# Optimization experiments

Hardware: AMD Instinct MI355X
Metric: run time of the kernel (lower is better)

The kernel has to match this reference:

```python
import jax, jax.numpy as jnp
import numpy as np

NQ = 4
NL = 3
HEADS = 8

_H = jnp.asarray(np.array([[1, 1], [1, -1]], np.complex64) / np.sqrt(2.0))
_X = jnp.asarray(np.array([[0, 1], [1, 0]], np.complex64))
_Y = jnp.asarray(np.array([[0, -1j], [1j, 0]], np.complex64))
_Z = jnp.asarray(np.array([[1, 0], [0, -1]], np.complex64))
_CNOT = jnp.asarray(np.array([[1, 0, 0, 0], [0, 1, 0, 0], [0, 0, 0, 1], [0, 0, 1, 0]], np.complex64))


def _rx(t):
    c = jnp.cos(t / 2).astype(jnp.complex64)
    s = (-1j * jnp.sin(t / 2)).astype(jnp.complex64)
    return jnp.stack([jnp.stack([c, s]), jnp.stack([s, c])])


def _ry(t):
    c = jnp.cos(t / 2).astype(jnp.complex64)
    s = jnp.sin(t / 2).astype(jnp.complex64)
    return jnp.stack([jnp.stack([c, -s]), jnp.stack([s, c])])


def _rz(t):
    e = jnp.exp((-0.5j) * t).astype(jnp.complex64)
    z = jnp.zeros((), jnp.complex64)
    return jnp.stack([jnp.stack([e, z]), jnp.stack([z, jnp.conj(e)])])


def _crx(t):
    # control-RX in |control,target> basis
    return jnp.eye(4, dtype=jnp.complex64).at[2:, 2:].set(_rx(t))


def _ap1(psi, U, q):
    # apply 2x2 gate U on qubit axis q of psi:(2,2,2,2)
    return jnp.moveaxis(jnp.tensordot(U, psi, axes=[[1], [q]]), 0, q)


def _ap2(psi, U, q1, q2):
    p = jnp.moveaxis(psi, (q1, q2), (0, 1)).reshape(4, 4)
    p = (U @ p).reshape(2, 2, 2, 2)
    return jnp.moveaxis(p, (0, 1), (q1, q2))


def _expv(psi, P, q):
    return jnp.real(jnp.vdot(psi, _ap1(psi, P, q)))


def _circuit(inp, w, ew, gam, bet):
    # inp:(4,)  w,ew:(3,4)  gam,bet:(3,)  -> (12,) expvals Z,X,Y
    psi = jnp.zeros((16,), jnp.complex64).at[0].set(1.0).reshape(2, 2, 2, 2)
    for i in range(NQ):  # AngleEmbedding(rotation='Y')
        psi = _ap1(psi, _ry(inp[i]), i)
    for L in range(NL):
        for i in range(NQ):
            psi = _ap1(psi, _rx(w[L, i]), i)
            psi = _ap1(psi, _ry(w[L, i]), i)
            psi = _ap1(psi, _rz(w[L, i]), i)
        for i in range(NQ):  # CRX entangling ring
            psi = _ap2(psi, _crx(ew[L, i]), i, (i + 1) % NQ)
        # Grover diffusion
        for q in range(NQ):
            psi = _ap1(psi, _H, q)
        for q in range(NQ):
            psi = _ap1(psi, _X, q)
        psi = _ap1(psi, _H, NQ - 1)
        psi = psi.at[1, 1, 1, :].set(psi[1, 1, 1, ::-1])  # CCCX ctrl=[0,1,2] tgt=3
        psi = _ap1(psi, _H, NQ - 1)
        for q in range(NQ):
            psi = _ap1(psi, _X, q)
        for q in range(NQ):
            psi = _ap1(psi, _H, q)
        # QAOA cost + mixer
        for i in range(NQ - 1):
            psi = _ap2(psi, _CNOT, i, i + 1)
            psi = _ap1(psi, _rz(gam[L]), i + 1)
            psi = _ap2(psi, _CNOT, i, i + 1)
        for q in range(NQ):
            psi = _ap1(psi, _rx(bet[L]), q)
    meas = [_expv(psi, _Z, q) for q in range(NQ)]
    meas += [_expv(psi, _X, q) for q in range(NQ)]
    meas += [_expv(psi, _Y, q) for q in range(NQ)]
    return jnp.stack(meas)


_vqc = jax.vmap(_circuit, in_axes=(0, None, None, None, None))


def _layernorm(x, g, b, eps=1e-5):
    mu = jnp.mean(x, -1, keepdims=True)
    var = jnp.mean((x - mu) ** 2, -1, keepdims=True)
    return (x - mu) * jax.lax.rsqrt(var + eps) * g + b


def _qtransform(xf, Wp, bp, ln_g, ln_b, w, ew, gam, bet):
    p = jnp.tanh(xf @ Wp.T + bp)  # (BS,4)
    p = _layernorm(p, ln_g, ln_b)
    return _vqc(p, w, ew, gam, bet)  # (BS,12)


def setup_inputs() -> dict:
    key = jax.random.key(0)
    ks = jax.random.split(key, 32)
    B, S, Hd = 4, 1024, 512
    d = {"x": jax.random.normal(ks[0], (B, S, Hd), jnp.float32)}
    d["Wp"] = jax.random.normal(ks[1], (NQ, Hd), jnp.float32) * 0.05
    d["bp"] = jnp.zeros((NQ,), jnp.float32)
    d["ln_g"] = jnp.ones((NQ,), jnp.float32)
    d["ln_b"] = jnp.zeros((NQ,), jnp.float32)
    i = 2
    for pfx in ["q", "k", "v"]:
        d[pfx + "w"] = 0.01 * jax.random.normal(ks[i], (NL, NQ), jnp.float32)
        d[pfx + "e"] = 0.01 * jax.random.normal(ks[i + 1], (NL, NQ), jnp.float32)
        d[pfx + "g"] = 0.01 * jax.random.normal(ks[i + 2], (NL,), jnp.float32)
        d[pfx + "b"] = 0.01 * jax.random.normal(ks[i + 3], (NL,), jnp.float32)
        i += 4
    fused = 3 * NQ
    d["Wq"] = jax.random.normal(ks[i], (Hd, fused), jnp.float32) * 0.2
    d["bq"] = jnp.zeros((Hd,), jnp.float32)
    d["Wk"] = jax.random.normal(ks[i + 1], (Hd, fused), jnp.float32) * 0.2
    d["bk"] = jnp.zeros((Hd,), jnp.float32)
    d["Wv"] = jax.random.normal(ks[i + 2], (Hd, fused), jnp.float32) * 0.2
    d["bv"] = jnp.zeros((Hd,), jnp.float32)
    d["Wo"] = jax.random.normal(ks[i + 3], (Hd, Hd), jnp.float32) * 0.05
    d["bo"] = jnp.zeros((Hd,), jnp.float32)
    return d


def reference(x, Wp, bp, ln_g, ln_b, qw, qe, qg, qb, kw, ke, kg, kb, vw, ve, vg, vb,
              Wq, bq, Wk, bk, Wv, bv, Wo, bo):
    B, S, Hd = x.shape
    hd = Hd // HEADS
    xf = x.reshape(B * S, Hd)
    tq = _qtransform(xf, Wp, bp, ln_g, ln_b, qw, qe, qg, qb)
    tk = _qtransform(xf, Wp, bp, ln_g, ln_b, kw, ke, kg, kb)
    tv = _qtransform(xf, Wp, bp, ln_g, ln_b, vw, ve, vg, vb)
    q = (tq @ Wq.T + bq).reshape(B, S, HEADS, hd)
    k = (tk @ Wk.T + bk).reshape(B, S, HEADS, hd)
    v = (tv @ Wv.T + bv).reshape(B, S, HEADS, hd)
    scale = float(hd) ** 0.5
    attn = jax.nn.softmax(jnp.einsum('bqhd,bkhd->bhqk', q, k) / scale, axis=-1)
    out = jnp.einsum('bhqk,bkhd->bqhd', attn, v).reshape(B, S, Hd)
    return out @ Wo.T + bo
```

## Files before the change

kernel.cpp:

```cpp
#include <hip/hip_runtime.h>
#include <hip/hip_bf16.h>
#include <math.h>

#define NROWS 4096
#define HD 512
#define HEADS 8
#define HDD 64
#define SEQ 1024
#define QSCALE 0.18033688011112042f

typedef unsigned short u16;
typedef __attribute__((ext_vector_type(8))) short sh8;
typedef __attribute__((ext_vector_type(4))) float f4;

__device__ __forceinline__ f4 mfma16(sh8 a, sh8 b, f4 c) {
  return __builtin_amdgcn_mfma_f32_16x16x32_bf16(a, b, c, 0, 0, 0);
}

__device__ __forceinline__ u16 f2bf(float x) {
  union { float f; unsigned u; } v; v.f = x;
  unsigned r = v.u + 0x7fff + ((v.u >> 16) & 1);
  return (u16)(r >> 16);
}

#define SWZA(r, cb) ((((r) * 128) + (cb)) ^ (((r) & 7) << 4))
#define SWZB(r, cb) ((((r) * 256) + (cb)) ^ (((r) & 7) << 4))

__global__ __launch_bounds__(256) void k_prep(
    const float* __restrict__ qw, const float* __restrict__ qe,
    const float* __restrict__ qg, const float* __restrict__ qb,
    const float* __restrict__ kw, const float* __restrict__ ke,
    const float* __restrict__ kg, const float* __restrict__ kb,
    const float* __restrict__ vw, const float* __restrict__ ve,
    const float* __restrict__ vg, const float* __restrict__ vb,
    float* __restrict__ Mout) {
  const int c = blockIdx.x;
  const int tid = threadIdx.x;
  __shared__ float aC[32], aS[32];
  __shared__ float GT[60][8];
  __shared__ int   GM[60][2];
  __shared__ float PF[3][16][2];
  __shared__ float SR[16][17], SI[16][17];
  __shared__ float TS[16], TI[16];
  __shared__ float Ur[256], Ui[256];

  const float* w = (c == 0) ? qw : (c == 1) ? kw : vw;
  const float* e = (c == 0) ? qe : (c == 1) ? ke : ve;
  const float* g = (c == 0) ? qg : (c == 1) ? kg : vg;
  const float* b = (c == 0) ? qb : (c == 1) ? kb : vb;

  if (tid < 30) {
    float ang = (tid < 12) ? w[tid] : (tid < 24) ? e[tid - 12]
               : (tid < 27) ? g[tid - 24] : b[tid - 27];
    float s_, c_;
    sincosf(0.5f * ang, &s_, &c_);
    aC[tid] = c_; aS[tid] = s_;
  }
  __syncthreads();

  if (tid < 60) {
    int L = tid / 20, s5 = tid % 20;
    int typ, aidx, M, C;
    if (s5 < 12) {
      int q = s5 / 3; typ = s5 % 3; aidx = L * 4 + q; M = 8 >> q; C = 0;
    } else if (s5 < 16) {
      int q = s5 - 12; typ = 0; aidx = 12 + L * 4 + q;
      C = 8 >> q; M = 8 >> ((q + 1) & 3);
    } else {
      int q = s5 - 16; typ = 0; aidx = 27 + L; M = 8 >> q; C = 0;
    }
    float cc = aC[aidx], ss = aS[aidx];
    float u0r = cc, u0i = 0.f, u1r = 0.f, u1i = 0.f,
          u2r = 0.f, u2i = 0.f, u3r = cc, u3i = 0.f;
    if (typ == 0)      { u1i = -ss; u2i = -ss; }
    else if (typ == 1) { u1r = -ss; u2r = ss; }
    else               { u0i = -ss; u3i = ss; }
    GT[tid][0] = u0r; GT[tid][1] = u0i; GT[tid][2] = u1r; GT[tid][3] = u1i;
    GT[tid][4] = u2r; GT[tid][5] = u2i; GT[tid][6] = u3r; GT[tid][7] = u3i;
    GM[tid][0] = M; GM[tid][1] = C;
  }
  if (tid >= 64 && tid < 112) {
    int idx = tid - 64, L = idx >> 4, a = idx & 15;
    float cg = aC[24 + L], sg = aS[24 + L];
    float c2 = cg * cg - sg * sg, s2 = 2.f * cg * sg;
    float c3 = cg * c2 - sg * s2, s3 = cg * s2 + sg * c2;
    int u = (a ^ (a >> 1)) & 7;
    int n = (u & 1) + ((u >> 1) & 1) + ((u >> 2) & 1);
    PF[L][a][0] = (n == 0 || n == 3) ? c3 : cg;
    PF[L][a][1] = (n == 0) ? -s3 : (n == 1) ? -sg : (n == 2) ? sg : s3;
  }
  for (int i = tid; i < 256; i += 256) {
    SR[i >> 4][i & 15] = (i >> 4) == (i & 15) ? 1.f : 0.f;
    SI[i >> 4][i & 15] = 0.f;
  }
  __syncthreads();

  const int p = tid >> 4, col = tid & 15;
  for (int L = 0; L < 3; ++L) {
    for (int s5 = 0; s5 < 16; ++s5) {
      if (tid < 128) {
        int gi = L * 20 + s5;
        const float* u = GT[gi];
        int M = GM[gi][0], C = GM[gi][1];
        int lo = p & (M - 1);
        int a = ((p - lo) << 1) | lo;
        int bb = a | M;
        bool act = (C == 0) | ((a & C) != 0);
        float ar = SR[a][col], ai = SI[a][col];
        float br = SR[bb][col], bi = SI[bb][col];
        float nar = u[0]*ar - u[1]*ai + u[2]*br - u[3]*bi;
        float nai = u[0]*ai + u[1]*ar + u[2]*bi + u[3]*br;
        float nbr = u[4]*ar - u[5]*ai + u[6]*br - u[7]*bi;
        float nbi = u[4]*ai + u[5]*ar + u[6]*bi + u[7]*br;
        SR[a][col]  = act ? nar : ar;  SI[a][col]  = act ? nai : ai;
        SR[bb][col] = act ? nbr : br;  SI[bb][col] = act ? nbi : bi;
      }
      __syncthreads();
    }
    if (tid < 16) {
      float sR = 0.f, sI = 0.f;
      for (int a = 0; a < 16; ++a) { sR += SR[a][tid]; sI += SI[a][tid]; }
      TS[tid] = sR * 0.125f; TI[tid] = sI * 0.125f;
    }
    __syncthreads();
    if (tid < 128) {
      for (int k = 0; k < 2; ++k) {
        int a = 2 * p + k;
        float vr = SR[a][col] - TS[col];
        float vi = SI[a][col] - TI[col];
        float pc = PF[L][a][0], ps = PF[L][a][1];
        SR[a][col] = vr * pc - vi * ps;
        SI[a][col] = vr * ps + vi * pc;
      }
    }
    __syncthreads();
    for (int s5 = 16; s5 < 20; ++s5) {
      if (tid < 128) {
        int gi = L * 20 + s5;
        const float* u = GT[gi];
        int M = GM[gi][0];
        int lo = p & (M - 1);
        int a = ((p - lo) << 1) | lo;
        int bb = a | M;
        float ar = SR[a][col], ai = SI[a][col];
        float br = SR[bb][col], bi = SI[bb][col];
        SR[a][col]  = u[0]*ar - u[1]*ai + u[2]*br - u[3]*bi;
        SI[a][col]  = u[0]*ai + u[1]*ar + u[2]*bi + u[3]*br;
        SR[bb][col] = u[4]*ar - u[5]*ai + u[6]*br - u[7]*bi;
        SI[bb][col] = u[4]*ai + u[5]*ar + u[6]*bi + u[7]*br;
      }
      __syncthreads();
    }
  }

  for (int i = tid; i < 256; i += 256) {
    Ur[i] = SR[i >> 4][i & 15];
    Ui[i] = SI[i >> 4][i & 15];
  }
  __syncthreads();

  if (tid < 192) {
    const int j = tid >> 4, a = tid & 15;
    const int typ = j >> 2;
    const int Mm = 8 >> (j & 3);
    float ax[4] = {0.f,0.f,0.f,0.f}, ay[4] = {0.f,0.f,0.f,0.f},
          az[4] = {0.f,0.f,0.f,0.f}, aw[4] = {0.f,0.f,0.f,0.f};
#pragma clang loop unroll_count(4)
    for (int k = 0; k < 16; ++k) {
      float uar = Ur[k * 16 + a], uai = Ui[k * 16 + a];
      int k2; float cR, cI;
      if (typ == 0)      { k2 = k;      float z = (k & Mm) ? -1.f : 1.f; cR = z*uar; cI = z*uai; }
      else if (typ == 1) { k2 = k ^ Mm; cR = uar; cI = uai; }
      else               { k2 = k ^ Mm; float sg = (k & Mm) ? 1.f : -1.f; cR = sg*uai; cI = -sg*uar; }
      const float* ur2 = Ur + k2 * 16;
      const float* ui2 = Ui + k2 * 16;
#pragma unroll
      for (int i = 0; i < 4; ++i) {
        ax[i] += cR * ur2[i*4+0] + cI * ui2[i*4+0];
        ay[i] += cR * ur2[i*4+1] + cI * ui2[i*4+1];
        az[i] += cR * ur2[i*4+2] + cI * ui2[i*4+2];
        aw[i] += cR * ur2[i*4+3] + cI * ui2[i*4+3];
      }
    }
    float* dst = Mout + ((c * 12 + j) * 16 + a) * 16;
#pragma unroll
    for (int i = 0; i < 4; ++i)
      ((float4*)dst)[i] = make_float4(ax[i], ay[i], az[i], aw[i]);
  }
}

__global__ __launch_bounds__(256) void k_fused(const float* __restrict__ x,
    const float* __restrict__ Wp, const float* __restrict__ bp,
    const float* __restrict__ ln_g, const float* __restrict__ ln_b,
    const float* __restrict__ Mg,
    const float* __restrict__ Wq, const float* __restrict__ bq,
    const float* __restrict__ Wk, const float* __restrict__ bk,
    const float* __restrict__ Wv, const float* __restrict__ bv,
    u16* __restrict__ Qo, u16* __restrict__ Ko, u16* __restrict__ Vto) {
  const int rb = blockIdx.x;
  const int tid = threadIdx.x;
  __shared__ float Ml[3][12][256];
  __shared__ float pl[16][4];
  __shared__ float psil[16][17];
  __shared__ float tt[3][16][12];

  {
    const float4* src = (const float4*)Mg;
    float4* dst = (float4*)&Ml[0][0][0];
    for (int i = tid; i < 2304; i += 256) dst[i] = src[i];
  }

  const int w = tid >> 6, lane = tid & 63;
  {
    float4 wpa[4], wpb[4];
#pragma unroll
    for (int j = 0; j < 4; ++j) {
      wpa[j] = *(const float4*)(Wp + j * HD + lane * 8);
      wpb[j] = *(const float4*)(Wp + j * HD + lane * 8 + 4);
    }
    for (int i = 0; i < 4; ++i) {
      int r = w * 4 + i;
      const float* xr = x + (rb * 16 + r) * HD + lane * 8;
      float4 xa = *(const float4*)xr, xb = *(const float4*)(xr + 4);
      float acc[4];
#pragma unroll
      for (int j = 0; j < 4; ++j)
        acc[j] = xa.x*wpa[j].x + xa.y*wpa[j].y + xa.z*wpa[j].z + xa.w*wpa[j].w
               + xb.x*wpb[j].x + xb.y*wpb[j].y + xb.z*wpb[j].z + xb.w*wpb[j].w;
#pragma unroll
      for (int j = 0; j < 4; ++j)
#pragma unroll
        for (int off = 32; off >= 1; off >>= 1)
          acc[j] += __shfl_xor(acc[j], off);
      if (lane == 0) {
        float v0 = tanhf(acc[0] + bp[0]);
        float v1 = tanhf(acc[1] + bp[1]);
        float v2 = tanhf(acc[2] + bp[2]);
        float v3 = tanhf(acc[3] + bp[3]);
        float mu = 0.25f * (v0 + v1 + v2 + v3);
        float d0 = v0 - mu, d1 = v1 - mu, d2 = v2 - mu, d3 = v3 - mu;
        float inv = rsqrtf(0.25f * (d0*d0 + d1*d1 + d2*d2 + d3*d3) + 1e-5f);
        pl[r][0] = d0 * inv * ln_g[0] + ln_b[0];
        pl[r][1] = d1 * inv * ln_g[1] + ln_b[1];
        pl[r][2] = d2 * inv * ln_g[2] + ln_b[2];
        pl[r][3] = d3 * inv * ln_g[3] + ln_b[3];
      }
    }
  }
  __syncthreads();

  if (tid < 16) {
    float cs[4], sn[4];
    sincosf(0.5f * pl[tid][0], &sn[0], &cs[0]);
    sincosf(0.5f * pl[tid][1], &sn[1], &cs[1]);
    sincosf(0.5f * pl[tid][2], &sn[2], &cs[2]);
    sincosf(0.5f * pl[tid][3], &sn[3], &cs[3]);
    float q01[4] = {cs[0]*cs[1], cs[0]*sn[1], sn[0]*cs[1], sn[0]*sn[1]};
    float q23[4] = {cs[2]*cs[3], cs[2]*sn[3], sn[2]*cs[3], sn[2]*sn[3]};
#pragma unroll
    for (int a = 0; a < 16; ++a) psil[tid][a] = q01[a >> 2] * q23[a & 3];
  }
  __syncthreads();

  if (tid < 192) {
    const int r = tid & 15, j = tid >> 4;
    float psi[16];
#pragma unroll
    for (int a = 0; a < 16; ++a) psi[a] = psil[r][a];
#pragma clang loop unroll(disable)
    for (int c = 0; c < 3; ++c) {
      const float* Mj = &Ml[c][j][0];
      float y = 0.f;
#pragma unroll
      for (int a = 0; a < 16; ++a) {
        float rsum = 0.f;
#pragma unroll
        for (int i = 0; i < 16; ++i) rsum += Mj[a*16+i] * psi[i];
        y += psi[a] * rsum;
      }
      tt[c][r][j] = y;
    }
  }
  __syncthreads();

  const int n0 = rb * 16, b = n0 >> 10, ss0 = n0 & 1023;
  {
    const int o0 = tid * 2;
    float wq0[12], wq1[12], wk0[12], wk1[12];
#pragma unroll
    for (int j = 0; j < 12; ++j) {
      wq0[j] = Wq[o0*12 + j];  wq1[j] = Wq[(o0+1)*12 + j];
      wk0[j] = Wk[o0*12 + j];  wk1[j] = Wk[(o0+1)*12 + j];
    }
    const float bq0 = bq[o0], bq1 = bq[o0+1], bk0 = bk[o0], bk1 = bk[o0+1];
    const int h = o0 >> 6, d = o0 & 63;
    u16* qrow = Qo + ((b * HEADS + h) * SEQ + ss0) * HDD + d;
    u16* krow = Ko + ((b * HEADS + h) * SEQ + ss0) * HDD + d;
    for (int rr = 0; rr < 16; ++rr) {
      float a0 = bq0, a1 = bq1, c0 = bk0, c1 = bk1;
#pragma unroll
      for (int j = 0; j < 12; ++j) {
        float tq = tt[0][rr][j], tk = tt[1][rr][j];
        a0 += tq * wq0[j]; a1 += tq * wq1[j];
        c0 += tk * wk0[j]; c1 += tk * wk1[j];
      }
      unsigned qv = (unsigned)f2bf(a0 * QSCALE) | ((unsigned)f2bf(a1 * QSCALE) << 16);
      unsigned kv = (unsigned)f2bf(c0) | ((unsigned)f2bf(c1) << 16);
      *(unsigned*)(qrow + rr * HDD) = qv;
      *(unsigned*)(krow + rr * HDD) = kv;
    }
  }
  {
    const int sp = tid & 7, gg = tid >> 3;
    const int r0 = 2 * sp, r1 = r0 + 1;
    for (int i = 0; i < 16; ++i) {
      int o = gg + 32 * i;
      float v0 = bv[o], v1 = bv[o];
#pragma unroll
      for (int j = 0; j < 12; ++j) {
        float wv = Wv[o * 12 + j];
        v0 += tt[2][r0][j] * wv;
        v1 += tt[2][r1][j] * wv;
      }
      unsigned vv = (unsigned)f2bf(v0) | ((unsigned)f2bf(v1) << 16);
      *(unsigned*)(Vto + (b * 512 + o) * SEQ + ss0 + r0) = vv;
    }
  }
}

__global__ __launch_bounds__(256) void k_attn_mfma(const u16* __restrict__ Q,
    const u16* __restrict__ K, const u16* __restrict__ Vt,
    u16* __restrict__ Ob) {
  const int bh = blockIdx.y, qt = blockIdx.x;
  const int tid = threadIdx.x, w = tid >> 6, l = tid & 63;
  const int lr = l & 15, lh = l >> 4;

  __shared__ u16 Kl[2][128 * 64];
  __shared__ u16 Vl[2][64 * 128];
  __shared__ u16 Pl[4][16 * 128];

  const u16* Qb = Q + (bh * SEQ + qt * 64) * HDD;
  const u16* Kb = K + bh * SEQ * HDD;
  const u16* Vb = Vt + bh * HDD * SEQ;

  sh8 qf[2];
#pragma unroll
  for (int kk = 0; kk < 2; ++kk)
    qf[kk] = *(const sh8*)(Qb + (w * 16 + lr) * HDD + kk * 32 + lh * 8);

  f4 oacc[4];
  float lsum[4] = {0.f, 0.f, 0.f, 0.f};
#pragma unroll
  for (int n = 0; n < 4; ++n) oacc[n] = (f4){0.f, 0.f, 0.f, 0.f};

  sh8 kreg[4], vreg[4];

#define STAGE_LOAD(ch) { \
    _Pragma("unroll") \
    for (int i = 0; i < 4; ++i) { \
      int idx = i * 256 + tid; \
      kreg[i] = *(const sh8*)(Kb + ((ch) * 128 + (idx >> 3)) * HDD + (idx & 7) * 8); \
      vreg[i] = *(const sh8*)(Vb + (idx >> 4) * SEQ + (ch) * 128 + (idx & 15) * 8); \
    } }
#define STAGE_WRITE(buf) { \
    _Pragma("unroll") \
    for (int i = 0; i < 4; ++i) { \
      int idx = i * 256 + tid; \
      *(sh8*)((char*)Kl[buf] + SWZA(idx >> 3, (idx & 7) * 16)) = kreg[i]; \
      *(sh8*)((char*)Vl[buf] + SWZB(idx >> 4, (idx & 15) * 16)) = vreg[i]; \
    } }

  STAGE_LOAD(0)
  STAGE_WRITE(0)
  __syncthreads();

  for (int ch = 0; ch < SEQ / 128; ++ch) {
    const int cur = ch & 1;
    if (ch < 7) STAGE_LOAD(ch + 1)

    f4 sacc[8];
#pragma unroll
    for (int n = 0; n < 8; ++n) sacc[n] = (f4){0.f, 0.f, 0.f, 0.f};
#pragma unroll
    for (int kk = 0; kk < 2; ++kk) {
#pragma unroll
      for (int n = 0; n < 8; ++n) {
        sh8 kf = *(const sh8*)((const char*)Kl[cur] + SWZA(n * 16 + lr, kk * 64 + lh * 16));
        sacc[n] = mfma16(qf[kk], kf, sacc[n]);
      }
    }

#pragma unroll
    for (int n = 0; n < 8; ++n) {
#pragma unroll
      for (int r = 0; r < 4; ++r) {
        float pv = exp2f(sacc[n][r]);
        lsum[r] += pv;
        *(u16*)((char*)Pl[w] + SWZB(lh * 4 + r, (n * 16 + lr) * 2)) = f2bf(pv);
      }
    }

#pragma unroll
    for (int kk = 0; kk < 4; ++kk) {
      sh8 pf = *(const sh8*)((const char*)Pl[w] + SWZB(lr, kk * 64 + lh * 16));
#pragma unroll
      for (int n = 0; n < 4; ++n) {
        sh8 vf = *(const sh8*)((const char*)Vl[cur] + SWZB(n * 16 + lr, kk * 64 + lh * 16));
        oacc[n] = mfma16(pf, vf, oacc[n]);
      }
    }

    if (ch < 7) STAGE_WRITE(cur ^ 1)
    __syncthreads();
  }
#undef STAGE_LOAD
#undef STAGE_WRITE

#pragma unroll
  for (int r = 0; r < 4; ++r) {
    lsum[r] += __shfl_xor(lsum[r], 1); lsum[r] += __shfl_xor(lsum[r], 2);
    lsum[r] += __shfl_xor(lsum[r], 4); lsum[r] += __shfl_xor(lsum[r], 8);
  }

  int bb = bh >> 3, h = bh & 7;
#pragma unroll
  for (int r = 0; r < 4; ++r) {
    int row = qt * 64 + w * 16 + lh * 4 + r;
    float inv = 1.f / lsum[r];
#pragma unroll
    for (int n = 0; n < 4; ++n)
      Ob[(bb * SEQ + row) * HD + h * 64 + n * 16 + lr] = f2bf(oacc[n][r] * inv);
  }
}

__global__ __launch_bounds__(256) void k_oproj_mfma(const u16* __restrict__ A,
    const float* __restrict__ W, const float* __restrict__ bo,
    float* __restrict__ out) {
  const int nb = blockIdx.x, ob = blockIdx.y;
  const int tid = threadIdx.x, w = tid >> 6, l = tid & 63;
  const int lr = l & 15, lh = l >> 4;
  __shared__ u16 Al[64 * 64];
  __shared__ u16 Wl[64 * 64];
  f4 acc[4];
#pragma unroll
  for (int n = 0; n < 4; ++n) acc[n] = (f4){0.f, 0.f, 0.f, 0.f};
  for (int ch = 0; ch < 8; ++ch) {
    __syncthreads();
#pragma unroll
    for (int i = 0; i < 2; ++i) {
      int idx = i * 256 + tid;
      int r = idx >> 3, c8 = idx & 7;
      *(sh8*)((char*)Al + SWZA(r, c8 * 16)) =
          *(const sh8*)(A + (nb * 64 + r) * HD + ch * 64 + c8 * 8);
      const float* wp = W + (ob * 64 + r) * HD + ch * 64 + c8 * 8;
      float4 f0 = *(const float4*)wp;
      float4 f1 = *(const float4*)(wp + 4);
      sh8 wv;
      wv[0] = (short)f2bf(f0.x); wv[1] = (short)f2bf(f0.y);
      wv[2] = (short)f2bf(f0.z); wv[3] = (short)f2bf(f0.w);
      wv[4] = (short)f2bf(f1.x); wv[5] = (short)f2bf(f1.y);
      wv[6] = (short)f2bf(f1.z); wv[7] = (short)f2bf(f1.w);
      *(sh8*)((char*)Wl + SWZA(r, c8 * 16)) = wv;
    }
    __syncthreads();
#pragma unroll
    for (int kk = 0; kk < 2; ++kk) {
      sh8 af = *(const sh8*)((const char*)Al + SWZA(w * 16 + lr, kk * 64 + lh * 16));
#pragma unroll
      for (int n = 0; n < 4; ++n) {
        sh8 wf = *(const sh8*)((const char*)Wl + SWZA(n * 16 + lr, kk * 64 + lh * 16));
        acc[n] = mfma16(af, wf, acc[n]);
      }
    }
  }
#pragma unroll
  for (int r = 0; r < 4; ++r) {
    int row = nb * 64 + w * 16 + lh * 4 + r;
#pragma unroll
    for (int n = 0; n < 4; ++n) {
      int col = ob * 64 + n * 16 + lr;
      out[row * HD + col] = acc[n][r] + bo[col];
    }
  }
}

extern "C" void kernel_launch(void* const* d_in, const int* in_sizes, int n_in,
                              void* d_out, int out_size, void* d_ws, size_t ws_size,
                              hipStream_t stream) {
  const float* x    = (const float*)d_in[0];
  const float* Wp   = (const float*)d_in[1];
  const float* bp   = (const float*)d_in[2];
  const float* ln_g = (const float*)d_in[3];
  const float* ln_b = (const float*)d_in[4];
  const float* qw   = (const float*)d_in[5];
  const float* qe   = (const float*)d_in[6];
  const float* qg   = (const float*)d_in[7];
  const float* qb_  = (const float*)d_in[8];
  const float* kw   = (const float*)d_in[9];
  const float* ke   = (const float*)d_in[10];
  const float* kg   = (const float*)d_in[11];
  const float* kb_  = (const float*)d_in[12];
  const float* vw   = (const float*)d_in[13];
  const float* ve   = (const float*)d_in[14];
  const float* vg   = (const float*)d_in[15];
  const float* vb_  = (const float*)d_in[16];
  const float* Wq   = (const float*)d_in[17];
  const float* bq   = (const float*)d_in[18];
  const float* Wk   = (const float*)d_in[19];
  const float* bk   = (const float*)d_in[20];
  const float* Wv   = (const float*)d_in[21];
  const float* bv   = (const float*)d_in[22];
  const float* Wo   = (const float*)d_in[23];
  const float* bo   = (const float*)d_in[24];

  float* ws   = (float*)d_ws;
  float* Mbuf = ws;
  u16* qb  = (u16*)(Mbuf + 9216);
  u16* kb  = qb + 32 * SEQ * HDD;
  u16* vtb = kb + 32 * SEQ * HDD;
  u16* ab  = vtb + 32 * SEQ * HDD;

  k_prep<<<3, 256, 0, stream>>>(qw, qe, qg, qb_, kw, ke, kg, kb_,
                                vw, ve, vg, vb_, Mbuf);
  k_fused<<<NROWS / 16, 256, 0, stream>>>(x, Wp, bp, ln_g, ln_b, Mbuf,
                                          Wq, bq, Wk, bk, Wv, bv, qb, kb, vtb);
  dim3 ga(SEQ / 64, 32);
  k_attn_mfma<<<ga, 256, 0, stream>>>(qb, kb, vtb, ab);
  dim3 go(NROWS / 64, HD / 64);
  k_oproj_mfma<<<go, 256, 0, stream>>>(ab, Wo, bo, (float*)d_out);
}
```

Before: 86.42 us.

## Shrink front-end row tiles and restructure attention to read K/V from global

The front kernel now handles 4 rows per block instead of 16. It reads the circuit matrices straight from global memory instead of staging 36KB in LDS, and spreads the 3 circuits across threads. Q/K/V projections use vectorized weight loads, and V is written as packed 64-bit stores. The attention kernel gives each wave 32 query rows (two 16-row MFMA tiles sharing K/V fragments), so the grid halves. It drops LDS double-buffering of K/V in favour of direct global/cache loads, separated only by sched barriers. This removes LDS staging and block syncs at the cost of more global/L2 traffic and higher register pressure.

```diff
diff --git a/kernel.cpp b/kernel.cpp
--- a/kernel.cpp
+++ b/kernel.cpp
@@ -10,6 +10,8 @@
 #define QSCALE 0.18033688011112042f
 
 typedef unsigned short u16;
+typedef unsigned int u32;
+typedef unsigned long long u64;
 typedef __attribute__((ext_vector_type(8))) short sh8;
 typedef __attribute__((ext_vector_type(4))) float f4;
 
@@ -189,7 +191,7 @@
   }
 }
 
-__global__ __launch_bounds__(256) void k_fused(const float* __restrict__ x,
+__global__ __launch_bounds__(256) void k_front(const float* __restrict__ x,
     const float* __restrict__ Wp, const float* __restrict__ bp,
     const float* __restrict__ ln_g, const float* __restrict__ ln_b,
     const float* __restrict__ Mg,
@@ -199,57 +201,44 @@
     u16* __restrict__ Qo, u16* __restrict__ Ko, u16* __restrict__ Vto) {
   const int rb = blockIdx.x;
   const int tid = threadIdx.x;
-  __shared__ float Ml[3][12][256];
-  __shared__ float pl[16][4];
-  __shared__ float psil[16][17];
-  __shared__ float tt[3][16][12];
+  const int w = tid >> 6, lane = tid & 63;
+  __shared__ float pl[4][4];
+  __shared__ float psil[4][16];
+  __shared__ float tt[3][4][12];
 
   {
-    const float4* src = (const float4*)Mg;
-    float4* dst = (float4*)&Ml[0][0][0];
-    for (int i = tid; i < 2304; i += 256) dst[i] = src[i];
-  }
-
-  const int w = tid >> 6, lane = tid & 63;
-  {
-    float4 wpa[4], wpb[4];
+    const float* xr = x + (rb * 4 + w) * HD + lane * 8;
+    float4 xa = *(const float4*)xr, xb = *(const float4*)(xr + 4);
+    float acc[4];
 #pragma unroll
     for (int j = 0; j < 4; ++j) {
-      wpa[j] = *(const float4*)(Wp + j * HD + lane * 8);
-      wpb[j] = *(const float4*)(Wp + j * HD + lane * 8 + 4);
-    }
-    for (int i = 0; i < 4; ++i) {
-      int r = w * 4 + i;
-      const float* xr = x + (rb * 16 + r) * HD + lane * 8;
-      float4 xa = *(const float4*)xr, xb = *(const float4*)(xr + 4);
-      float acc[4];
-#pragma unroll
-      for (int j = 0; j < 4; ++j)
-        acc[j] = xa.x*wpa[j].x + xa.y*wpa[j].y + xa.z*wpa[j].z + xa.w*wpa[j].w
-               + xb.x*wpb[j].x + xb.y*wpb[j].y + xb.z*wpb[j].z + xb.w*wpb[j].w;
-#pragma unroll
-      for (int j = 0; j < 4; ++j)
-#pragma unroll
-        for (int off = 32; off >= 1; off >>= 1)
-          acc[j] += __shfl_xor(acc[j], off);
-      if (lane == 0) {
-        float v0 = tanhf(acc[0] + bp[0]);
-        float v1 = tanhf(acc[1] + bp[1]);
-        float v2 = tanhf(acc[2] + bp[2]);
-        float v3 = tanhf(acc[3] + bp[3]);
-        float mu = 0.25f * (v0 + v1 + v2 + v3);
-        float d0 = v0 - mu, d1 = v1 - mu, d2 = v2 - mu, d3 = v3 - mu;
-        float inv = rsqrtf(0.25f * (d0*d0 + d1*d1 + d2*d2 + d3*d3) + 1e-5f);
-        pl[r][0] = d0 * inv * ln_g[0] + ln_b[0];
-        pl[r][1] = d1 * inv * ln_g[1] + ln_b[1];
-        pl[r][2] = d2 * inv * ln_g[2] + ln_b[2];
-        pl[r][3] = d3 * inv * ln_g[3] + ln_b[3];
-      }
+      const float* wr = Wp + j * HD + lane * 8;
+      float4 wa = *(const float4*)wr, wb = *(const float4*)(wr + 4);
+      acc[j] = xa.x*wa.x + xa.y*wa.y + xa.z*wa.z + xa.w*wa.w
+             + xb.x*wb.x + xb.y*wb.y + xb.z*wb.z + xb.w*wb.w;
+    }
+#pragma unroll
+    for (int j = 0; j < 4; ++j)
+#pragma unroll
+      for (int off = 32; off >= 1; off >>= 1)
+        acc[j] += __shfl_xor(acc[j], off);
+    if (lane == 0) {
+      float v0 = tanhf(acc[0] + bp[0]);
+      float v1 = tanhf(acc[1] + bp[1]);
+      float v2 = tanhf(acc[2] + bp[2]);
+      float v3 = tanhf(acc[3] + bp[3]);
+      float mu = 0.25f * (v0 + v1 + v2 + v3);
+      float d0 = v0 - mu, d1 = v1 - mu, d2 = v2 - mu, d3 = v3 - mu;
+      float inv = rsqrtf(0.25f * (d0*d0 + d1*d1 + d2*d2 + d3*d3) + 1e-5f);
+      pl[w][0] = d0 * inv * ln_g[0] + ln_b[0];
+      pl[w][1] = d1 * inv * ln_g[1] + ln_b[1];
+      pl[w][2] = d2 * inv * ln_g[2] + ln_b[2];
+      pl[w][3] = d3 * inv * ln_g[3] + ln_b[3];
     }
   }
   __syncthreads();
 
-  if (tid < 16) {
+  if (tid < 4) {
     float cs[4], sn[4];
     sincosf(0.5f * pl[tid][0], &sn[0], &cs[0]);
     sincosf(0.5f * pl[tid][1], &sn[1], &cs[1]);
@@ -262,175 +251,169 @@
   }
   __syncthreads();
 
-  if (tid < 192) {
-    const int r = tid & 15, j = tid >> 4;
+  if (tid < 144) {
+    const int c = tid / 48, rem = tid - c * 48, j = rem >> 2, r = rem & 3;
     float psi[16];
 #pragma unroll
     for (int a = 0; a < 16; ++a) psi[a] = psil[r][a];
-#pragma clang loop unroll(disable)
-    for (int c = 0; c < 3; ++c) {
-      const float* Mj = &Ml[c][j][0];
-      float y = 0.f;
-#pragma unroll
-      for (int a = 0; a < 16; ++a) {
-        float rsum = 0.f;
-#pragma unroll
-        for (int i = 0; i < 16; ++i) rsum += Mj[a*16+i] * psi[i];
-        y += psi[a] * rsum;
-      }
-      tt[c][r][j] = y;
-    }
+    const float4* Mj = (const float4*)(Mg + (c * 12 + j) * 256);
+    float y = 0.f;
+#pragma unroll
+    for (int a = 0; a < 16; ++a) {
+      float rsum = 0.f;
+#pragma unroll
+      for (int i = 0; i < 4; ++i) {
+        float4 m4 = Mj[a * 4 + i];
+        rsum += m4.x*psi[i*4] + m4.y*psi[i*4+1] + m4.z*psi[i*4+2] + m4.w*psi[i*4+3];
+      }
+      y += psi[a] * rsum;
+    }
+    tt[c][r][j] = y;
   }
   __syncthreads();
 
-  const int n0 = rb * 16, b = n0 >> 10, ss0 = n0 & 1023;
-  {
-    const int o0 = tid * 2;
-    float wq0[12], wq1[12], wk0[12], wk1[12];
-#pragma unroll
-    for (int j = 0; j < 12; ++j) {
-      wq0[j] = Wq[o0*12 + j];  wq1[j] = Wq[(o0+1)*12 + j];
-      wk0[j] = Wk[o0*12 + j];  wk1[j] = Wk[(o0+1)*12 + j];
-    }
-    const float bq0 = bq[o0], bq1 = bq[o0+1], bk0 = bk[o0], bk1 = bk[o0+1];
-    const int h = o0 >> 6, d = o0 & 63;
-    u16* qrow = Qo + ((b * HEADS + h) * SEQ + ss0) * HDD + d;
-    u16* krow = Ko + ((b * HEADS + h) * SEQ + ss0) * HDD + d;
-    for (int rr = 0; rr < 16; ++rr) {
-      float a0 = bq0, a1 = bq1, c0 = bk0, c1 = bk1;
-#pragma unroll
-      for (int j = 0; j < 12; ++j) {
-        float tq = tt[0][rr][j], tk = tt[1][rr][j];
-        a0 += tq * wq0[j]; a1 += tq * wq1[j];
-        c0 += tk * wk0[j]; c1 += tk * wk1[j];
-      }
-      unsigned qv = (unsigned)f2bf(a0 * QSCALE) | ((unsigned)f2bf(a1 * QSCALE) << 16);
-      unsigned kv = (unsigned)f2bf(c0) | ((unsigned)f2bf(c1) << 16);
-      *(unsigned*)(qrow + rr * HDD) = qv;
-      *(unsigned*)(krow + rr * HDD) = kv;
-    }
-  }
-  {
-    const int sp = tid & 7, gg = tid >> 3;
-    const int r0 = 2 * sp, r1 = r0 + 1;
-    for (int i = 0; i < 16; ++i) {
-      int o = gg + 32 * i;
-      float v0 = bv[o], v1 = bv[o];
-#pragma unroll
-      for (int j = 0; j < 12; ++j) {
-        float wv = Wv[o * 12 + j];
-        v0 += tt[2][r0][j] * wv;
-        v1 += tt[2][r1][j] * wv;
-      }
-      unsigned vv = (unsigned)f2bf(v0) | ((unsigned)f2bf(v1) << 16);
-      *(unsigned*)(Vto + (b * 512 + o) * SEQ + ss0 + r0) = vv;
-    }
-  }
-}
-
-__global__ __launch_bounds__(256) void k_attn_mfma(const u16* __restrict__ Q,
+  const int o0 = tid * 2;
+  const int b = rb >> 8, ss0 = (rb & 255) * 4;
+  const int h = o0 >> 6, d = o0 & 63;
+#pragma unroll
+  for (int c = 0; c < 3; ++c) {
+    const float* W  = (c == 0) ? Wq : (c == 1) ? Wk : Wv;
+    const float* bb = (c == 0) ? bq : (c == 1) ? bk : bv;
+    float4 w0a = *(const float4*)(W + o0 * 12);
+    float4 w0b = *(const float4*)(W + o0 * 12 + 4);
+    float4 w0c = *(const float4*)(W + o0 * 12 + 8);
+    float4 w1a = *(const float4*)(W + o0 * 12 + 12);
+    float4 w1b = *(const float4*)(W + o0 * 12 + 16);
+    float4 w1c = *(const float4*)(W + o0 * 12 + 20);
+    float b0 = bb[o0], b1 = bb[o0 + 1];
+    float r0[4], r1[4];
+#pragma unroll
+    for (int r = 0; r < 4; ++r) {
+      const float* t = tt[c][r];
+      r0[r] = b0 + t[0]*w0a.x + t[1]*w0a.y + t[2]*w0a.z + t[3]*w0a.w
+                 + t[4]*w0b.x + t[5]*w0b.y + t[6]*w0b.z + t[7]*w0b.w
+                 + t[8]*w0c.x + t[9]*w0c.y + t[10]*w0c.z + t[11]*w0c.w;
+      r1[r] = b1 + t[0]*w1a.x + t[1]*w1a.y + t[2]*w1a.z + t[3]*w1a.w
+                 + t[4]*w1b.x + t[5]*w1b.y + t[6]*w1b.z + t[7]*w1b.w
+                 + t[8]*w1c.x + t[9]*w1c.y + t[10]*w1c.z + t[11]*w1c.w;
+    }
+    if (c == 0) {
+      u16* qrow = Qo + ((b * HEADS + h) * SEQ + ss0) * HDD + d;
+#pragma unroll
+      for (int r = 0; r < 4; ++r)
+        *(u32*)(qrow + r * HDD) =
+            (u32)f2bf(r0[r] * QSCALE) | ((u32)f2bf(r1[r] * QSCALE) << 16);
+    } else if (c == 1) {
+      u16* krow = Ko + ((b * HEADS + h) * SEQ + ss0) * HDD + d;
+#pragma unroll
+      for (int r = 0; r < 4; ++r)
+        *(u32*)(krow + r * HDD) = (u32)f2bf(r0[r]) | ((u32)f2bf(r1[r]) << 16);
+    } else {
+      u64 v0 = (u64)((u32)f2bf(r0[0]) | ((u32)f2bf(r0[1]) << 16)) |
+               ((u64)((u32)f2bf(r0[2]) | ((u32)f2bf(r0[3]) << 16)) << 32);
+      u64 v1 = (u64)((u32)f2bf(r1[0]) | ((u32)f2bf(r1[1]) << 16)) |
+               ((u64)((u32)f2bf(r1[2]) | ((u32)f2bf(r1[3]) << 16)) << 32);
+      *(u64*)(Vto + (b * 512 + o0) * SEQ + ss0) = v0;
+      *(u64*)(Vto + (b * 512 + o0 + 1) * SEQ + ss0) = v1;
+    }
+  }
+}
+
+__global__ __launch_bounds__(256) void k_attn(const u16* __restrict__ Q,
     const u16* __restrict__ K, const u16* __restrict__ Vt,
     u16* __restrict__ Ob) {
   const int bh = blockIdx.y, qt = blockIdx.x;
   const int tid = threadIdx.x, w = tid >> 6, l = tid & 63;
   const int lr = l & 15, lh = l >> 4;
 
-  __shared__ u16 Kl[2][128 * 64];
-  __shared__ u16 Vl[2][64 * 128];
-  __shared__ u16 Pl[4][16 * 128];
-
-  const u16* Qb = Q + (bh * SEQ + qt * 64) * HDD;
+  __shared__ u16 Pl[4][32 * 128];
+
+  const u16* Qb = Q + (bh * SEQ + qt * 128 + w * 32) * HDD;
   const u16* Kb = K + bh * SEQ * HDD;
   const u16* Vb = Vt + bh * HDD * SEQ;
-
-  sh8 qf[2];
-#pragma unroll
-  for (int kk = 0; kk < 2; ++kk)
-    qf[kk] = *(const sh8*)(Qb + (w * 16 + lr) * HDD + kk * 32 + lh * 8);
-
-  f4 oacc[4];
-  float lsum[4] = {0.f, 0.f, 0.f, 0.f};
-#pragma unroll
-  for (int n = 0; n < 4; ++n) oacc[n] = (f4){0.f, 0.f, 0.f, 0.f};
-
-  sh8 kreg[4], vreg[4];
-
-#define STAGE_LOAD(ch) { \
-    _Pragma("unroll") \
-    for (int i = 0; i < 4; ++i) { \
-      int idx = i * 256 + tid; \
-      kreg[i] = *(const sh8*)(Kb + ((ch) * 128 + (idx >> 3)) * HDD + (idx & 7) * 8); \
-      vreg[i] = *(const sh8*)(Vb + (idx >> 4) * SEQ + (ch) * 128 + (idx & 15) * 8); \
-    } }
-#define STAGE_WRITE(buf) { \
-    _Pragma("unroll") \
-    for (int i = 0; i < 4; ++i) { \
-      int idx = i * 256 + tid; \
-      *(sh8*)((char*)Kl[buf] + SWZA(idx >> 3, (idx & 7) * 16)) = kreg[i]; \
-      *(sh8*)((char*)Vl[buf] + SWZB(idx >> 4, (idx & 15) * 16)) = vreg[i]; \
-    } }
-
-  STAGE_LOAD(0)
-  STAGE_WRITE(0)
-  __syncthreads();
+  u16* Plw = Pl[w];
+
+  sh8 qf[2][2];
+#pragma unroll
+  for (int m = 0; m < 2; ++m)
+#pragma unroll
+    for (int kk = 0; kk < 2; ++kk)
+      qf[m][kk] = *(const sh8*)(Qb + (m * 16 + lr) * HDD + kk * 32 + lh * 8);
+
+  f4 oacc[2][4];
+  float lsum[2][4];
+#pragma unroll
+  for (int m = 0; m < 2; ++m)
+#pragma unroll
+    for (int n = 0; n < 4; ++n) oacc[m][n] = (f4){0.f, 0.f, 0.f, 0.f};
+#pragma unroll
+  for (int m = 0; m < 2; ++m)
+#pragma unroll
+    for (int r = 0; r < 4; ++r) lsum[m][r] = 0.f;
 
   for (int ch = 0; ch < SEQ / 128; ++ch) {
-    const int cur = ch & 1;
-    if (ch < 7) STAGE_LOAD(ch + 1)
-
-    f4 sacc[8];
-#pragma unroll
-    for (int n = 0; n < 8; ++n) sacc[n] = (f4){0.f, 0.f, 0.f, 0.f};
+    f4 sacc[2][8];
+#pragma unroll
+    for (int m = 0; m < 2; ++m)
+#pragma unroll
+      for (int n = 0; n < 8; ++n) sacc[m][n] = (f4){0.f, 0.f, 0.f, 0.f};
 #pragma unroll
     for (int kk = 0; kk < 2; ++kk) {
 #pragma unroll
       for (int n = 0; n < 8; ++n) {
-        sh8 kf = *(const sh8*)((const char*)Kl[cur] + SWZA(n * 16 + lr, kk * 64 + lh * 16));
-        sacc[n] = mfma16(qf[kk], kf, sacc[n]);
-      }
-    }
-
-#pragma unroll
-    for (int n = 0; n < 8; ++n) {
-#pragma unroll
-      for (int r = 0; r < 4; ++r) {
-        float pv = exp2f(sacc[n][r]);
-        lsum[r] += pv;
-        *(u16*)((char*)Pl[w] + SWZB(lh * 4 + r, (n * 16 + lr) * 2)) = f2bf(pv);
-      }
-    }
+        sh8 kf = *(const sh8*)(Kb + (ch * 128 + n * 16 + lr) * HDD + kk * 32 + lh * 8);
+        sacc[0][n] = mfma16(qf[0][kk], kf, sacc[0][n]);
+        sacc[1][n] = mfma16(qf[1][kk], kf, sacc[1][n]);
+      }
+    }
+
+#pragma unroll
+    for (int m = 0; m < 2; ++m)
+#pragma unroll
+      for (int n = 0; n < 8; ++n)
+#pragma unroll
+        for (int r = 0; r < 4; ++r) {
+          float pv = exp2f(sacc[m][n][r]);
+          lsum[m][r] += pv;
+          *(u16*)((char*)Plw + SWZB(m * 16 + lh * 4 + r, (n * 16 + lr) * 2)) = f2bf(pv);
+        }
+    __builtin_amdgcn_sched_barrier(0);
 
 #pragma unroll
     for (int kk = 0; kk < 4; ++kk) {
-      sh8 pf = *(const sh8*)((const char*)Pl[w] + SWZB(lr, kk * 64 + lh * 16));
+      sh8 pf0 = *(const sh8*)((const char*)Plw + SWZB(lr,      kk * 64 + lh * 16));
+      sh8 pf1 = *(const sh8*)((const char*)Plw + SWZB(16 + lr, kk * 64 + lh * 16));
 #pragma unroll
       for (int n = 0; n < 4; ++n) {
-        sh8 vf = *(const sh8*)((const char*)Vl[cur] + SWZB(n * 16 + lr, kk * 64 + lh * 16));
-        oacc[n] = mfma16(pf, vf, oacc[n]);
-      }
-    }
-
-    if (ch < 7) STAGE_WRITE(cur ^ 1)
-    __syncthreads();
-  }
-#undef STAGE_LOAD
-#undef STAGE_WRITE
-
-#pragma unroll
-  for (int r = 0; r < 4; ++r) {
-    lsum[r] += __shfl_xor(lsum[r], 1); lsum[r] += __shfl_xor(lsum[r], 2);
-    lsum[r] += __shfl_xor(lsum[r], 4); lsum[r] += __shfl_xor(lsum[r], 8);
-  }
-
-  int bb = bh >> 3, h = bh & 7;
-#pragma unroll
-  for (int r = 0; r < 4; ++r) {
-    int row = qt * 64 + w * 16 + lh * 4 + r;
-    float inv = 1.f / lsum[r];
-#pragma unroll
-    for (int n = 0; n < 4; ++n)
-      Ob[(bb * SEQ + row) * HD + h * 64 + n * 16 + lr] = f2bf(oacc[n][r] * inv);
-  }
+        sh8 vf = *(const sh8*)(Vb + (n * 16 + lr) * SEQ + ch * 128 + kk * 32 + lh * 8);
+        oacc[0][n] = mfma16(pf0, vf, oacc[0][n]);
+        oacc[1][n] = mfma16(pf1, vf, oacc[1][n]);
+      }
+    }
+    __builtin_amdgcn_sched_barrier(0);
+  }
+
+#pragma unroll
+  for (int m = 0; m < 2; ++m)
+#pragma unroll
+    for (int r = 0; r < 4; ++r) {
+      float s = lsum[m][r];
+      s += __shfl_xor(s, 1); s += __shfl_xor(s, 2);
+      s += __shfl_xor(s, 4); s += __shfl_xor(s, 8);
+      lsum[m][r] = s;
+    }
+
+  const int bb = bh >> 3, h = bh & 7;
+#pragma unroll
+  for (int m = 0; m < 2; ++m)
+#pragma unroll
+    for (int r = 0; r < 4; ++r) {
+      int row = qt * 128 + w * 32 + m * 16 + lh * 4 + r;
+      float inv = 1.f / lsum[m][r];
+#pragma unroll
+      for (int n = 0; n < 4; ++n)
+        Ob[(bb * SEQ + row) * HD + h * 64 + n * 16 + lr] = f2bf(oacc[m][n][r] * inv);
+    }
 }
 
 __global__ __launch_bounds__(256) void k_oproj_mfma(const u16* __restrict__ A,
@@ -522,10 +505,10 @@
 
   k_prep<<<3, 256, 0, stream>>>(qw, qe, qg, qb_, kw, ke, kg, kb_,
                                 vw, ve, vg, vb_, Mbuf);
-  k_fused<<<NROWS / 16, 256, 0, stream>>>(x, Wp, bp, ln_g, ln_b, Mbuf,
-                                          Wq, bq, Wk, bk, Wv, bv, qb, kb, vtb);
-  dim3 ga(SEQ / 64, 32);
-  k_attn_mfma<<<ga, 256, 0, stream>>>(qb, kb, vtb, ab);
+  k_front<<<NROWS / 4, 256, 0, stream>>>(x, Wp, bp, ln_g, ln_b, Mbuf,
+                                         Wq, bq, Wk, bk, Wv, bv, qb, kb, vtb);
+  dim3 ga(SEQ / 128, 32);
+  k_attn<<<ga, 256, 0, stream>>>(qb, kb, vtb, ab);
   dim3 go(NROWS / 64, HD / 64);
   k_oproj_mfma<<<go, 256, 0, stream>>>(ab, Wo, bo, (float*)d_out);
 }
```

New measurement: 126.8 us. 46.7% more time.
